# Performance work log

Hardware: AMD Instinct MI355X
Metric: run time of the kernel (lower is better)

Reference implementation:

```python
import jax, jax.numpy as jnp
import numpy as np

B, S, D, H, HD = 2, 2048, 2048, 16, 128
MAX_TIMESCALE = 10000.0


def _fixed_pos_embedding(features, length, max_timescale):
    # flaxformer embedding.generate_fixed_pos_embedding
    fraction = jnp.arange(0, features, 2, dtype=jnp.float32) / features
    timescale = max_timescale ** fraction  # min_timescale = 1.0
    sinusoid = jnp.einsum('i,j->ij', jnp.arange(length, dtype=jnp.float32), 1.0 / timescale)
    sinusoid = jnp.concatenate([sinusoid, sinusoid], axis=-1)  # [length, features]
    return jnp.sin(sinusoid), jnp.cos(sinusoid)


def _rotate_half(x):
    x1, x2 = jnp.split(x, 2, axis=-1)
    return jnp.concatenate([-x2, x1], axis=-1)


def _apply_rope(x, sin, cos):
    # x: [B, S, H, HD]; sin/cos: [S, HD]
    sin = sin[None, :, None, :].astype(x.dtype)
    cos = cos[None, :, None, :].astype(x.dtype)
    return x * cos + _rotate_half(x) * sin


def setup_inputs() -> dict:
    key = jax.random.key(0)
    ks = jax.random.split(key, 6)
    inputs_q = jax.random.normal(ks[0], (B, S, D), dtype=jnp.float32)
    inputs_kv = jax.random.normal(ks[1], (B, S, D), dtype=jnp.float32)
    scale = D ** -0.5
    wq = jax.random.normal(ks[2], (D, H, HD), dtype=jnp.float32) * scale
    wk = jax.random.normal(ks[3], (D, H, HD), dtype=jnp.float32) * scale
    wv = jax.random.normal(ks[4], (D, H, HD), dtype=jnp.float32) * scale
    wo = jax.random.normal(ks[5], (H, HD, D), dtype=jnp.float32) * ((H * HD) ** -0.5)
    mask = jnp.tril(jnp.ones((S, S), dtype=bool))[None, None]  # causal [1,1,S,S]
    return {"inputs_q": inputs_q, "inputs_kv": inputs_kv, "wq": wq, "wk": wk,
            "wv": wv, "wo": wo, "mask": mask}


def reference(inputs_q, inputs_kv, wq, wk, wv, wo, mask):
    # QKV projections (split-head kernels) -> [B, S, H, HD]
    q = jnp.einsum('bqd,dhf->bqhf', inputs_q, wq)
    k = jnp.einsum('bkd,dhf->bkhf', inputs_kv, wk)
    v = jnp.einsum('bkd,dhf->bkhf', inputs_kv, wv)

    # Rotary embeddings applied to full head dim (fraction_to_rotate = 1.0)
    sin, cos = _fixed_pos_embedding(HD, S, MAX_TIMESCALE)
    q = _apply_rope(q, sin, cos)
    k = _apply_rope(k, sin, cos)

    # Logit rescaling by 1/sqrt(head_dim) (rescale_logits=False default path)
    q = q * (HD ** -0.5)

    logits = jnp.einsum('bqhf,bkhf->bhqk', q, k)  # [B, H, S, S]
    logits = jnp.where(mask, logits, jnp.asarray(-1e10, logits.dtype))
    probs = jax.nn.softmax(logits, axis=-1)

    ctx = jnp.einsum('bhqk,bkhf->bqhf', probs, v)
    out = jnp.einsum('bqhf,hfd->bqd', ctx, wo)  # output projection
    return out
```

## Files before the change

### kernel.cpp

```cpp
#include <hip/hip_runtime.h>

#define S_LEN 2048
#define NH 16
#define HDIM 128
#define DMODEL 2048

typedef __attribute__((ext_vector_type(8))) short bf16x8;
typedef __attribute__((ext_vector_type(4))) float f32x4;

using gas_cvp = const __attribute__((address_space(1))) void*;
using las_vp  = __attribute__((address_space(3))) void*;

__device__ __forceinline__ unsigned short f2bf(float x) {
  unsigned int u = __builtin_bit_cast(unsigned int, x);
  u += 0x7FFFu + ((u >> 16) & 1u);
  return (unsigned short)(u >> 16);
}
__device__ __forceinline__ float bf2f(unsigned short u) {
  unsigned int x = ((unsigned int)u) << 16;
  return __builtin_bit_cast(float, x);
}
__device__ __forceinline__ unsigned int cvt_pk_bf16(float lo, float hi) {
  unsigned int r;
  asm("v_cvt_pk_bf16_f32 %0, %1, %2" : "=v"(r) : "v"(lo), "v"(hi));
  return r;
}

__global__ __launch_bounds__(256) void cvt_kernel(const float4* __restrict__ in,
                                                  ushort4* __restrict__ out, int n4) {
  int i = blockIdx.x * 256 + threadIdx.x;
  if (i < n4) {
    float4 v = in[i];
    ushort4 r;
    r.x = f2bf(v.x); r.y = f2bf(v.y); r.z = f2bf(v.z); r.w = f2bf(v.w);
    out[i] = r;
  }
}

__global__ __launch_bounds__(256) void sincos_kernel(float2* __restrict__ sc) {
  int i = blockIdx.x * 256 + threadIdx.x;
  int s = i >> 6, j = i & 63;
  float inv_ts = 1.0f / powf(10000.0f, (float)j * (1.0f / 64.0f));
  float ang = (float)s * inv_ts;
  sc[i] = make_float2(sinf(ang), cosf(ang));
}

__global__ __launch_bounds__(256) void rope8_kernel(const unsigned short* __restrict__ XQ,
                                                    const unsigned short* __restrict__ XK,
                                                    const float2* __restrict__ sc,
                                                    unsigned short* __restrict__ outQ,
                                                    unsigned short* __restrict__ outK,
                                                    float qscale) {
  const unsigned short* X = blockIdx.z ? XK : XQ;
  unsigned short* out = blockIdx.z ? outK : outQ;
  float scale = blockIdx.z ? 1.0f : qscale;
  int i = blockIdx.x * 256 + threadIdx.x;
  int m = i >> 7;
  int r = i & 127;
  int h = r >> 3, jb = (r & 7) * 8;
  int s = m & (S_LEN - 1);
  size_t base = (size_t)m * DMODEL + h * HDIM + jb;
  int4 x1 = *(const int4*)(X + base);
  int4 x2 = *(const int4*)(X + base + 64);
  const float2* pp = sc + s * 64 + jb;
  int4 o1, o2;
  int* x1w = (int*)&x1; int* x2w = (int*)&x2;
  int* o1w = (int*)&o1; int* o2w = (int*)&o2;
#pragma unroll
  for (int w = 0; w < 4; w++) {
    float a_lo = bf2f((unsigned short)(x1w[w] & 0xffff));
    float a_hi = bf2f((unsigned short)((unsigned int)x1w[w] >> 16));
    float b_lo = bf2f((unsigned short)(x2w[w] & 0xffff));
    float b_hi = bf2f((unsigned short)((unsigned int)x2w[w] >> 16));
    float2 c0 = pp[w * 2], c1 = pp[w * 2 + 1];
    float r1l = (a_lo * c0.y - b_lo * c0.x) * scale;
    float r1h = (a_hi * c1.y - b_hi * c1.x) * scale;
    float r2l = (b_lo * c0.y + a_lo * c0.x) * scale;
    float r2h = (b_hi * c1.y + a_hi * c1.x) * scale;
    o1w[w] = (int)(cvt_pk_bf16(r1l, r1h));
    o2w[w] = (int)(cvt_pk_bf16(r2l, r2h));
  }
  *(int4*)(out + base) = o1;
  *(int4*)(out + base + 64) = o2;
}

__global__ __launch_bounds__(256) void wtrans4_kernel(const float* __restrict__ w0,
                                                      const float* __restrict__ w1,
                                                      const float* __restrict__ w2,
                                                      const float* __restrict__ w3,
                                                      unsigned short* __restrict__ outb) {
  __shared__ float tile[64][65];
  int z = blockIdx.z;
  const float* in = (z == 0) ? w0 : (z == 1) ? w1 : (z == 2) ? w2 : w3;
  unsigned short* out = outb + (size_t)z * DMODEL * DMODEL;
  int c0 = blockIdx.x * 64, r0 = blockIdx.y * 64;
  int tx = threadIdx.x & 63, ty = threadIdx.x >> 6;
#pragma unroll
  for (int i = 0; i < 16; i++) {
    int r = ty + i * 4;
    tile[r][tx] = in[(size_t)(r0 + r) * DMODEL + c0 + tx];
  }
  __syncthreads();
#pragma unroll
  for (int i = 0; i < 16; i++) {
    int c = ty + i * 4;
    out[(size_t)(c0 + c) * DMODEL + r0 + tx] = f2bf(tile[tx][c]);
  }
}

__global__ __launch_bounds__(256) void vtrans_kernel(const unsigned short* __restrict__ vf,
                                                     unsigned short* __restrict__ Vt) {
  __shared__ unsigned short tile[64][65];
  int z = blockIdx.z; int b = z >> 4, h = z & 15;
  const unsigned short* I = vf + (size_t)b * S_LEN * DMODEL + h * HDIM;
  unsigned short* O = Vt + (size_t)z * HDIM * S_LEN;
  int s0 = blockIdx.y * 64, f0 = blockIdx.x * 64;
  int tx = threadIdx.x & 63, ty = threadIdx.x >> 6;
#pragma unroll
  for (int i = 0; i < 16; i++) {
    int r = ty + i * 4;
    tile[r][tx] = I[(size_t)(s0 + r) * DMODEL + f0 + tx];
  }
  __syncthreads();
#pragma unroll
  for (int i = 0; i < 16; i++) {
    int c = ty + i * 4;
    O[(size_t)(f0 + c) * S_LEN + s0 + tx] = tile[tx][c];
  }
}

template <bool BF16OUT>
__global__ __launch_bounds__(512, 2) void gemm256_kernel(
    const unsigned short* __restrict__ Aq,
    const unsigned short* __restrict__ Akv,
    const unsigned short* __restrict__ W,
    void* __restrict__ Cb) {
  constexpr int M = 4096, N = 2048, K = 2048, NT = K / 64;
  __shared__ char lds[131072];
  int z = blockIdx.z;
  const unsigned short* A = (z == 0) ? Aq : Akv;
  const unsigned short* Bt = W + (size_t)z * N * K;

  int wid = blockIdx.y * 8 + blockIdx.x;
  int nid = (wid & 7) * 16 + (wid >> 3);
  int bn = (nid & 7) * 256, bm = (nid >> 3) * 256;

  int tid = threadIdx.x, wave = tid >> 6, lane = tid & 63;
  int lr = lane & 15, lq = lane >> 4;
  int wr = wave >> 2, wc = wave & 3;

  auto STAGE_Q = [&](int t, int buf, int isB, int q) {
    int k0 = (t & (NT - 1)) * 64;
    const unsigned short* src = isB ? Bt : A;
    int rbase = (isB ? bn : bm) + q * 64;
    int o = tid * 16;
    int row = o >> 7, colb = o & 127;
    int sc = colb ^ ((row & 7) << 4);
    __builtin_amdgcn_global_load_lds(
        (gas_cvp)(src + (size_t)(rbase + row) * K + k0 + (sc >> 1)),
        (las_vp)(lds + buf * 65536 + isB * 32768 + (q >> 1) * 16384 + (q & 1) * 8192 + wave * 1024),
        16, 0, 0);
  };
  auto STAGE_AA = [&](int t, int buf) { STAGE_Q(t, buf, 0, 0); STAGE_Q(t, buf, 0, 2); };
  auto STAGE_BIG = [&](int t, int buf) {
    STAGE_Q(t, buf, 0, 1); STAGE_Q(t, buf, 0, 3);
    STAGE_Q(t, buf, 1, 0); STAGE_Q(t, buf, 1, 1);
    STAGE_Q(t, buf, 1, 2); STAGE_Q(t, buf, 1, 3);
  };

  auto LDA = [&](int buf, int m, int kk) -> bf16x8 {
    int row = wr * 128 + m * 16 + lr;
    int half = row >> 7, r = row & 127;
    return *(const bf16x8*)(lds + buf * 65536 + half * 16384 + r * 128 +
                            (((kk * 4 + lq) ^ (r & 7)) << 4));
  };
  auto LDB = [&](int buf, int n, int kk) -> bf16x8 {
    int row = wc * 64 + n * 16 + lr;
    int half = row >> 7, r = row & 127;
    return *(const bf16x8*)(lds + buf * 65536 + 32768 + half * 16384 + r * 128 +
                            (((kk * 4 + lq) ^ (r & 7)) << 4));
  };

  f32x4 acc[8][4] = {};
  bf16x8 aA[4][2], bB[4][2];

  auto DS_A = [&](int buf, int mg) {
#pragma unroll
    for (int kk = 0; kk < 2; kk++)
#pragma unroll
      for (int mm = 0; mm < 4; mm++) aA[mm][kk] = LDA(buf, mg * 4 + mm, kk);
  };
  auto DS_B = [&](int buf, int ng) {
#pragma unroll
    for (int kk = 0; kk < 2; kk++)
#pragma unroll
      for (int nn = 0; nn < 2; nn++) bB[ng * 2 + nn][kk] = LDB(buf, ng * 2 + nn, kk);
  };
  auto MFMA_Q = [&](int mg, int ng) {
#pragma unroll
    for (int kk = 0; kk < 2; kk++)
#pragma unroll
      for (int mm = 0; mm < 4; mm++)
#pragma unroll
        for (int nn = 0; nn < 2; nn++)
          acc[mg * 4 + mm][ng * 2 + nn] = __builtin_amdgcn_mfma_f32_16x16x32_bf16(
              aA[mm][kk], bB[ng * 2 + nn][kk], acc[mg * 4 + mm][ng * 2 + nn], 0, 0, 0);
  };
  auto PH_MID = [&]() {
    __builtin_amdgcn_s_barrier();
    asm volatile("s_waitcnt lgkmcnt(0)" ::: "memory");
    __builtin_amdgcn_sched_barrier(0);
    __builtin_amdgcn_s_setprio(1);
  };
  auto PH_ENDP = [&]() {
    __builtin_amdgcn_s_setprio(0);
    __builtin_amdgcn_s_barrier();
  };
  auto PH_END_VM2 = [&]() {
    __builtin_amdgcn_s_setprio(0);
    asm volatile("s_waitcnt vmcnt(2)" ::: "memory");
    __builtin_amdgcn_sched_barrier(0);
    __builtin_amdgcn_s_barrier();
  };

  STAGE_AA(0, 0); STAGE_BIG(0, 0);
  STAGE_AA(1, 1);
  asm volatile("s_waitcnt vmcnt(2)" ::: "memory");
  __builtin_amdgcn_sched_barrier(0);
  __builtin_amdgcn_s_barrier();

  for (int i = 0; i < NT / 2; i++) {
    int T = 2 * i, U = T + 1;
    int t2 = (T + 2) & (NT - 1), u2 = (U + 2) & (NT - 1);
    DS_A(0, 0); DS_B(0, 0);
    STAGE_BIG(U, 1);
    PH_MID(); MFMA_Q(0, 0); PH_ENDP();
    DS_B(0, 1);
    PH_MID(); MFMA_Q(0, 1); PH_ENDP();
    DS_A(0, 1);
    STAGE_AA(t2, 0);
    PH_MID(); MFMA_Q(1, 0); PH_ENDP();
    PH_MID(); MFMA_Q(1, 1); PH_END_VM2();
    DS_A(1, 0); DS_B(1, 0);
    STAGE_BIG(t2, 0);
    PH_MID(); MFMA_Q(0, 0); PH_ENDP();
    DS_B(1, 1);
    PH_MID(); MFMA_Q(0, 1); PH_ENDP();
    DS_A(1, 1);
    STAGE_AA(u2, 1);
    PH_MID(); MFMA_Q(1, 0); PH_ENDP();
    PH_MID(); MFMA_Q(1, 1); PH_END_VM2();
  }
  asm volatile("s_waitcnt vmcnt(0)" ::: "memory");

#pragma unroll
  for (int m = 0; m < 8; m++)
#pragma unroll
    for (int n = 0; n < 4; n++) {
      int row0 = bm + wr * 128 + m * 16 + lq * 4;
      int col = bn + wc * 64 + n * 16 + lr;
      if (BF16OUT) {
        unsigned short* C = (unsigned short*)Cb + (size_t)z * M * N;
#pragma unroll
        for (int r = 0; r < 4; r++)
          C[(size_t)(row0 + r) * N + col] = f2bf(acc[m][n][r]);
      } else {
        float* C = (float*)Cb + (size_t)z * M * N;
#pragma unroll
        for (int r = 0; r < 4; r++)
          C[(size_t)(row0 + r) * N + col] = acc[m][n][r];
      }
    }
}

__global__ __launch_bounds__(512, 1) void attn_kernel(const unsigned short* __restrict__ Qb,
                                                      const unsigned short* __restrict__ Kb,
                                                      const unsigned short* __restrict__ Vt,
                                                      unsigned short* __restrict__ ctx) {
  __shared__ char lds[65536];
  int d = blockIdx.x + 8 * (blockIdx.y + 16 * blockIdx.z);
  int jlo = (d >> 3) & 7;
  int hb = (d & 7) * 4 + (d >> 6);
  int h = hb & 15, b = hb >> 4;

  int tid = threadIdx.x, wave = tid >> 6, lane = tid & 63;
  int lr = lane & 15, lq = lane >> 4;
  int grp = wave >> 2, wsub = wave & 3;
  int qtile = grp ? (15 - jlo) : jlo;
  int qw = qtile * 128 + wsub * 32;
  int nt = 2 * (15 - jlo) + 2;

  const unsigned short* Qp = Qb + (size_t)b * S_LEN * DMODEL + (size_t)h * HDIM;
  const unsigned short* Kp = Kb + (size_t)b * S_LEN * DMODEL + (size_t)h * HDIM;
  const unsigned short* Vp = Vt + (size_t)(b * NH + h) * HDIM * S_LEN;

  bf16x8 qa[2][4];
#pragma unroll
  for (int mi = 0; mi < 2; mi++)
#pragma unroll
    for (int kf = 0; kf < 4; kf++)
      qa[mi][kf] = *(const bf16x8*)(Qp + (size_t)(qw + mi * 16 + lr) * DMODEL + kf * 32 + lq * 8);

  f32x4 o[2][8] = {};
  float mrow[2] = {-1e30f, -1e30f};
  float lsum[2] = {0.f, 0.f};

  auto STAGE = [&](int tt, int bsel) {
    int kk0 = tt * 64;
#pragma unroll
    for (int i = 0; i < 2; i++) {
      int o_ = wave * 2048 + i * 1024 + lane * 16;
      int row = o_ >> 8, colb = o_ & 255;
      int sc_ = colb ^ ((row & 7) << 4);
      __builtin_amdgcn_global_load_lds(
          (gas_cvp)(Kp + (size_t)(kk0 + row) * DMODEL + (sc_ >> 1)),
          (las_vp)(lds + bsel * 32768 + wave * 2048 + i * 1024), 16, 0, 0);
    }
#pragma unroll
    for (int i = 0; i < 2; i++) {
      int o_ = wave * 2048 + i * 1024 + lane * 16;
      int row = o_ >> 7, colb = o_ & 127;
      int sc_ = colb ^ ((row & 7) << 4);
      __builtin_amdgcn_global_load_lds(
          (gas_cvp)(Vp + (size_t)row * S_LEN + kk0 + (sc_ >> 1)),
          (las_vp)(lds + bsel * 32768 + 16384 + wave * 2048 + i * 1024), 16, 0, 0);
    }
  };

  STAGE(0, 0);
  __syncthreads();

  for (int t = 0; t < nt; t++) {
    int cur = t & 1;
    int k0 = t * 64;
    if (t + 1 < nt) STAGE(t + 1, cur ^ 1);

    bool active = (k0 <= qw + 31);
    if (active) {
      const char* kbb = lds + cur * 32768;
      f32x4 sf[2][4] = {};
#pragma unroll
      for (int kf = 0; kf < 4; kf++) {
        bf16x8 kbf[4];
#pragma unroll
        for (int nf = 0; nf < 4; nf++) {
          int row = nf * 16 + lr;
          int colb = kf * 64 + lq * 16;
          kbf[nf] = *(const bf16x8*)(kbb + row * 256 + (colb ^ ((row & 7) << 4)));
        }
#pragma unroll
        for (int nf = 0; nf < 4; nf++)
#pragma unroll
          for (int mi = 0; mi < 2; mi++)
            sf[mi][nf] = __builtin_amdgcn_mfma_f32_16x16x32_bf16(kbf[nf], qa[mi][kf], sf[mi][nf], 0, 0, 0);
      }

      if (k0 + 63 > qw) {
#pragma unroll
        for (int mi = 0; mi < 2; mi++) {
          int q = qw + mi * 16 + lr;
#pragma unroll
          for (int nf = 0; nf < 4; nf++)
#pragma unroll
            for (int r = 0; r < 4; r++)
              if (k0 + nf * 16 + lq * 4 + r > q) sf[mi][nf][r] = -1e30f;
        }
      }

      float vmax[2];
#pragma unroll
      for (int mi = 0; mi < 2; mi++) {
        float v = sf[mi][0][0];
#pragma unroll
        for (int nf = 0; nf < 4; nf++)
#pragma unroll
          for (int r = 0; r < 4; r++) v = fmaxf(v, sf[mi][nf][r]);
        v = fmaxf(v, __shfl_xor(v, 16));
        v = fmaxf(v, __shfl_xor(v, 32));
        vmax[mi] = v;
      }
      bool need = (vmax[0] > mrow[0] + 8.f) || (vmax[1] > mrow[1] + 8.f);
      if (__any(need)) {
#pragma unroll
        for (int mi = 0; mi < 2; mi++) {
          float mn = fmaxf(mrow[mi], vmax[mi]);
          float al = __expf(mrow[mi] - mn);
          mrow[mi] = mn;
          lsum[mi] *= al;
#pragma unroll
          for (int ff = 0; ff < 8; ff++) o[mi][ff] *= al;
        }
      }
#pragma unroll
      for (int mi = 0; mi < 2; mi++) {
        float rs = 0.f;
#pragma unroll
        for (int nf = 0; nf < 4; nf++)
#pragma unroll
          for (int r = 0; r < 4; r++) {
            float p = __expf(sf[mi][nf][r] - mrow[mi]);
            sf[mi][nf][r] = p;
            rs += p;
          }
        rs += __shfl_xor(rs, 16);
        rs += __shfl_xor(rs, 32);
        lsum[mi] += rs;
      }

      const char* vbb = lds + cur * 32768 + 16384;
      bool hi = (lane >= 32);
      bool odd = (lq & 1);
#pragma unroll
      for (int c = 0; c < 2; c++) {
        bf16x8 pfrag[2];
#pragma unroll
        for (int mi = 0; mi < 2; mi++) {
          unsigned int A0 = cvt_pk_bf16(sf[mi][2 * c][0], sf[mi][2 * c][1]);
          unsigned int A1 = cvt_pk_bf16(sf[mi][2 * c][2], sf[mi][2 * c][3]);
          unsigned int B0 = cvt_pk_bf16(sf[mi][2 * c + 1][0], sf[mi][2 * c + 1][1]);
          unsigned int B1 = cvt_pk_bf16(sf[mi][2 * c + 1][2], sf[mi][2 * c + 1][3]);
          unsigned int sA0 = (unsigned int)__shfl_xor((int)A0, 32);
          unsigned int sA1 = (unsigned int)__shfl_xor((int)A1, 32);
          unsigned int sB0 = (unsigned int)__shfl_xor((int)B0, 32);
          unsigned int sB1 = (unsigned int)__shfl_xor((int)B1, 32);
          unsigned int Y0f = hi ? sB0 : A0, Y0s = hi ? B0 : sA0;
          unsigned int Y1f = hi ? sB1 : A1, Y1s = hi ? B1 : sA1;
          unsigned int z0 = odd ? Y0f : Y0s, z1 = odd ? Y1f : Y1s;
          unsigned int w0 = (unsigned int)__shfl_xor((int)z0, 16);
          unsigned int w1 = (unsigned int)__shfl_xor((int)z1, 16);
          int4 fr;
          fr.x = (int)(odd ? w0 : Y0f);
          fr.y = (int)(odd ? w1 : Y1f);
          fr.z = (int)(odd ? Y0s : w0);
          fr.w = (int)(odd ? Y1s : w1);
          pfrag[mi] = __builtin_bit_cast(bf16x8, fr);
        }
#pragma unroll
        for (int ff = 0; ff < 8; ff++) {
          int row = ff * 16 + lr;
          int colb = c * 64 + lq * 16;
          bf16x8 vb = *(const bf16x8*)(vbb + row * 128 + (colb ^ ((row & 7) << 4)));
#pragma unroll
          for (int mi = 0; mi < 2; mi++)
            o[mi][ff] = __builtin_amdgcn_mfma_f32_16x16x32_bf16(vb, pfrag[mi], o[mi][ff], 0, 0, 0);
        }
      }
    }

    __syncthreads();
  }

#pragma unroll
  for (int mi = 0; mi < 2; mi++) {
    float inv = 1.0f / lsum[mi];
    size_t rb = ((size_t)b * S_LEN + qw + mi * 16 + lr) * DMODEL + h * HDIM;
#pragma unroll
    for (int ff = 0; ff < 8; ff++) {
      unsigned int u0 = cvt_pk_bf16(o[mi][ff][0] * inv, o[mi][ff][1] * inv);
      unsigned int u1 = cvt_pk_bf16(o[mi][ff][2] * inv, o[mi][ff][3] * inv);
      *(uint2*)(ctx + rb + ff * 16 + lq * 4) = make_uint2(u0, u1);
    }
  }
}

extern "C" void kernel_launch(void* const* d_in, const int* in_sizes, int n_in,
                              void* d_out, int out_size, void* d_ws, size_t ws_size,
                              hipStream_t stream) {
  const float* inq  = (const float*)d_in[0];
  const float* inkv = (const float*)d_in[1];
  const float* wq   = (const float*)d_in[2];
  const float* wk   = (const float*)d_in[3];
  const float* wv   = (const float*)d_in[4];
  const float* wo   = (const float*)d_in[5];
  float* out = (float*)d_out;

  char* ws = (char*)d_ws;
  const size_t MB = 1ull << 20;
  unsigned short* xq  = (unsigned short*)(ws);
  unsigned short* xkv = (unsigned short*)(ws + 16 * MB);
  unsigned short* wqt = (unsigned short*)(ws + 32 * MB);
  unsigned short* wot = (unsigned short*)(ws + 56 * MB);
  float2* sc          = (float2*)(ws + 64 * MB);
  unsigned short* projb = (unsigned short*)(ws + 66 * MB);
  unsigned short* Vt   = (unsigned short*)(ws + 114 * MB);
  unsigned short* ctxb = (unsigned short*)(ws + 130 * MB);
  unsigned short* Qb = xq;
  unsigned short* Kb = xkv;

  const int n4 = (2 * S_LEN * DMODEL) / 4;
  cvt_kernel<<<n4 / 256, 256, 0, stream>>>((const float4*)inq, (ushort4*)xq, n4);
  cvt_kernel<<<n4 / 256, 256, 0, stream>>>((const float4*)inkv, (ushort4*)xkv, n4);

  wtrans4_kernel<<<dim3(32, 32, 4), 256, 0, stream>>>(wq, wk, wv, wo, wqt);

  sincos_kernel<<<(S_LEN * 64) / 256, 256, 0, stream>>>(sc);

  const float qscale = 0.08838834764831845f;
  unsigned short* projQ = projb;
  unsigned short* projK = projb + (size_t)4096 * 2048;
  unsigned short* projV = projb + (size_t)2 * 4096 * 2048;

  gemm256_kernel<true><<<dim3(8, 16, 3), 512, 0, stream>>>(xq, xkv, wqt, (void*)projb);

  rope8_kernel<<<dim3(2048, 1, 2), 256, 0, stream>>>(projQ, projK, sc, Qb, Kb, qscale);
  vtrans_kernel<<<dim3(2, 32, 32), 256, 0, stream>>>(projV, Vt);

  attn_kernel<<<dim3(8, NH, 2), 512, 0, stream>>>(Qb, Kb, Vt, ctxb);

  gemm256_kernel<false><<<dim3(8, 16, 1), 512, 0, stream>>>(ctxb, ctxb, wot, (void*)out);
}
```

Baseline: 302.0 us.

## Switch projection GEMMs to 256x128 tiles with 4-wave ping-pong pipeline

```diff
diff --git a/kernel.cpp b/kernel.cpp
--- a/kernel.cpp
+++ b/kernel.cpp
@@ -130,73 +130,75 @@
 }
 
 template <bool BF16OUT>
-__global__ __launch_bounds__(512, 2) void gemm256_kernel(
+__global__ __launch_bounds__(256, 1) void gemmp_kernel(
     const unsigned short* __restrict__ Aq,
     const unsigned short* __restrict__ Akv,
     const unsigned short* __restrict__ W,
     void* __restrict__ Cb) {
   constexpr int M = 4096, N = 2048, K = 2048, NT = K / 64;
-  __shared__ char lds[131072];
+  __shared__ char lds[98304];
   int z = blockIdx.z;
   const unsigned short* A = (z == 0) ? Aq : Akv;
   const unsigned short* Bt = W + (size_t)z * N * K;
 
-  int wid = blockIdx.y * 8 + blockIdx.x;
-  int nid = (wid & 7) * 16 + (wid >> 3);
-  int bn = (nid & 7) * 256, bm = (nid >> 3) * 256;
+  int wid = blockIdx.y * 16 + blockIdx.x;
+  int nid = (wid & 7) * 32 + (wid >> 3);
+  int bn = (nid & 15) * 128, bm = (nid >> 4) * 256;
 
   int tid = threadIdx.x, wave = tid >> 6, lane = tid & 63;
   int lr = lane & 15, lq = lane >> 4;
-  int wr = wave >> 2, wc = wave & 3;
-
-  auto STAGE_Q = [&](int t, int buf, int isB, int q) {
+  int wr = wave >> 1, wc = wave & 1;
+
+  auto STAGE_A_MG = [&](int t, int buf, int mg) {
     int k0 = (t & (NT - 1)) * 64;
-    const unsigned short* src = isB ? Bt : A;
-    int rbase = (isB ? bn : bm) + q * 64;
-    int o = tid * 16;
-    int row = o >> 7, colb = o & 127;
-    int sc = colb ^ ((row & 7) << 4);
-    __builtin_amdgcn_global_load_lds(
-        (gas_cvp)(src + (size_t)(rbase + row) * K + k0 + (sc >> 1)),
-        (las_vp)(lds + buf * 65536 + isB * 32768 + (q >> 1) * 16384 + (q & 1) * 8192 + wave * 1024),
-        16, 0, 0);
+#pragma unroll
+    for (int i = 0; i < 4; i++) {
+      int o = i * 4096 + wave * 1024 + lane * 16;
+      int rr = o >> 7, colb = o & 127;
+      int sc = colb ^ ((rr & 7) << 4);
+      int grow = bm + ((rr >> 6) << 7) + mg * 64 + (rr & 63);
+      __builtin_amdgcn_global_load_lds(
+          (gas_cvp)(A + (size_t)grow * K + k0 + (sc >> 1)),
+          (las_vp)(lds + buf * 49152 + mg * 16384 + i * 4096 + wave * 1024), 16, 0, 0);
+    }
   };
-  auto STAGE_AA = [&](int t, int buf) { STAGE_Q(t, buf, 0, 0); STAGE_Q(t, buf, 0, 2); };
-  auto STAGE_BIG = [&](int t, int buf) {
-    STAGE_Q(t, buf, 0, 1); STAGE_Q(t, buf, 0, 3);
-    STAGE_Q(t, buf, 1, 0); STAGE_Q(t, buf, 1, 1);
-    STAGE_Q(t, buf, 1, 2); STAGE_Q(t, buf, 1, 3);
+  auto STAGE_B = [&](int t, int buf) {
+    int k0 = (t & (NT - 1)) * 64;
+#pragma unroll
+    for (int i = 0; i < 4; i++) {
+      int o = i * 4096 + wave * 1024 + lane * 16;
+      int rr = o >> 7, colb = o & 127;
+      int sc = colb ^ ((rr & 7) << 4);
+      __builtin_amdgcn_global_load_lds(
+          (gas_cvp)(Bt + (size_t)(bn + rr) * K + k0 + (sc >> 1)),
+          (las_vp)(lds + buf * 49152 + 32768 + i * 4096 + wave * 1024), 16, 0, 0);
+    }
   };
 
-  auto LDA = [&](int buf, int m, int kk) -> bf16x8 {
-    int row = wr * 128 + m * 16 + lr;
-    int half = row >> 7, r = row & 127;
-    return *(const bf16x8*)(lds + buf * 65536 + half * 16384 + r * 128 +
-                            (((kk * 4 + lq) ^ (r & 7)) << 4));
+  bf16x8 aS0[4][2], aS1[4][2], bS0[2][2], bS1[2][2];
+  f32x4 acc[8][4] = {};
+
+  auto RD_A = [&](int buf, int mg, bf16x8 (&dst)[4][2]) {
+#pragma unroll
+    for (int kk = 0; kk < 2; kk++)
+#pragma unroll
+      for (int mm = 0; mm < 4; mm++) {
+        int rr = wr * 64 + mm * 16 + lr;
+        dst[mm][kk] = *(const bf16x8*)(lds + buf * 49152 + mg * 16384 + rr * 128 +
+                                       (((kk * 4 + lq) ^ (rr & 7)) << 4));
+      }
   };
-  auto LDB = [&](int buf, int n, int kk) -> bf16x8 {
-    int row = wc * 64 + n * 16 + lr;
-    int half = row >> 7, r = row & 127;
-    return *(const bf16x8*)(lds + buf * 65536 + 32768 + half * 16384 + r * 128 +
-                            (((kk * 4 + lq) ^ (r & 7)) << 4));
+  auto RD_Bn = [&](int buf, int ng, bf16x8 (&dst)[2][2]) {
+#pragma unroll
+    for (int kk = 0; kk < 2; kk++)
+#pragma unroll
+      for (int nn = 0; nn < 2; nn++) {
+        int rr = wc * 64 + (ng * 2 + nn) * 16 + lr;
+        dst[nn][kk] = *(const bf16x8*)(lds + buf * 49152 + 32768 + rr * 128 +
+                                       (((kk * 4 + lq) ^ (rr & 7)) << 4));
+      }
   };
-
-  f32x4 acc[8][4] = {};
-  bf16x8 aA[4][2], bB[4][2];
-
-  auto DS_A = [&](int buf, int mg) {
-#pragma unroll
-    for (int kk = 0; kk < 2; kk++)
-#pragma unroll
-      for (int mm = 0; mm < 4; mm++) aA[mm][kk] = LDA(buf, mg * 4 + mm, kk);
-  };
-  auto DS_B = [&](int buf, int ng) {
-#pragma unroll
-    for (int kk = 0; kk < 2; kk++)
-#pragma unroll
-      for (int nn = 0; nn < 2; nn++) bB[ng * 2 + nn][kk] = LDB(buf, ng * 2 + nn, kk);
-  };
-  auto MFMA_Q = [&](int mg, int ng) {
+  auto MFMA_Q = [&](int mg, int ng, bf16x8 (&aS)[4][2], bf16x8 (&bS)[2][2]) {
 #pragma unroll
     for (int kk = 0; kk < 2; kk++)
 #pragma unroll
@@ -204,54 +206,48 @@
 #pragma unroll
         for (int nn = 0; nn < 2; nn++)
           acc[mg * 4 + mm][ng * 2 + nn] = __builtin_amdgcn_mfma_f32_16x16x32_bf16(
-              aA[mm][kk], bB[ng * 2 + nn][kk], acc[mg * 4 + mm][ng * 2 + nn], 0, 0, 0);
+              aS[mm][kk], bS[nn][kk], acc[mg * 4 + mm][ng * 2 + nn], 0, 0, 0);
   };
-  auto PH_MID = [&]() {
+
+  STAGE_A_MG(0, 0, 0); STAGE_A_MG(0, 0, 1); STAGE_B(0, 0);
+  STAGE_B(1, 1);
+  asm volatile("s_waitcnt vmcnt(4)" ::: "memory");
+  __builtin_amdgcn_sched_barrier(0);
+  __builtin_amdgcn_s_barrier();
+  RD_A(0, 0, aS0); RD_Bn(0, 0, bS0);
+  __builtin_amdgcn_sched_barrier(0);
+
+  for (int X = 0; X < NT; X++) {
+    int c = X & 1, nc = c ^ 1;
+    RD_Bn(c, 1, bS1);
+    __builtin_amdgcn_sched_barrier(0);
+    STAGE_A_MG(X + 1, nc, 0);
+    asm volatile("s_waitcnt lgkmcnt(4)" ::: "memory");
+    __builtin_amdgcn_sched_barrier(0);
+    MFMA_Q(0, 0, aS0, bS0);
+    __builtin_amdgcn_s_barrier();
+    RD_A(c, 1, aS1);
+    __builtin_amdgcn_sched_barrier(0);
+    STAGE_A_MG(X + 1, nc, 1);
+    asm volatile("s_waitcnt lgkmcnt(8)" ::: "memory");
+    __builtin_amdgcn_sched_barrier(0);
+    MFMA_Q(0, 1, aS0, bS1);
     __builtin_amdgcn_s_barrier();
     asm volatile("s_waitcnt lgkmcnt(0)" ::: "memory");
     __builtin_amdgcn_sched_barrier(0);
-    __builtin_amdgcn_s_setprio(1);
-  };
-  auto PH_ENDP = [&]() {
-    __builtin_amdgcn_s_setprio(0);
+    MFMA_Q(1, 0, aS1, bS0);
+    asm volatile("s_waitcnt vmcnt(4)" ::: "memory");
+    __builtin_amdgcn_sched_barrier(0);
     __builtin_amdgcn_s_barrier();
-  };
-  auto PH_END_VM2 = [&]() {
-    __builtin_amdgcn_s_setprio(0);
-    asm volatile("s_waitcnt vmcnt(2)" ::: "memory");
+    RD_A(nc, 0, aS0); RD_Bn(nc, 0, bS0);
+    __builtin_amdgcn_sched_barrier(0);
+    STAGE_B(X + 2, c);
+    MFMA_Q(1, 1, aS1, bS1);
+    asm volatile("s_waitcnt vmcnt(4)" ::: "memory");
     __builtin_amdgcn_sched_barrier(0);
     __builtin_amdgcn_s_barrier();
-  };
-
-  STAGE_AA(0, 0); STAGE_BIG(0, 0);
-  STAGE_AA(1, 1);
-  asm volatile("s_waitcnt vmcnt(2)" ::: "memory");
-  __builtin_amdgcn_sched_barrier(0);
-  __builtin_amdgcn_s_barrier();
-
-  for (int i = 0; i < NT / 2; i++) {
-    int T = 2 * i, U = T + 1;
-    int t2 = (T + 2) & (NT - 1), u2 = (U + 2) & (NT - 1);
-    DS_A(0, 0); DS_B(0, 0);
-    STAGE_BIG(U, 1);
-    PH_MID(); MFMA_Q(0, 0); PH_ENDP();
-    DS_B(0, 1);
-    PH_MID(); MFMA_Q(0, 1); PH_ENDP();
-    DS_A(0, 1);
-    STAGE_AA(t2, 0);
-    PH_MID(); MFMA_Q(1, 0); PH_ENDP();
-    PH_MID(); MFMA_Q(1, 1); PH_END_VM2();
-    DS_A(1, 0); DS_B(1, 0);
-    STAGE_BIG(t2, 0);
-    PH_MID(); MFMA_Q(0, 0); PH_ENDP();
-    DS_B(1, 1);
-    PH_MID(); MFMA_Q(0, 1); PH_ENDP();
-    DS_A(1, 1);
-    STAGE_AA(u2, 1);
-    PH_MID(); MFMA_Q(1, 0); PH_ENDP();
-    PH_MID(); MFMA_Q(1, 1); PH_END_VM2();
-  }
-  asm volatile("s_waitcnt vmcnt(0)" ::: "memory");
+  }
+  asm volatile("s_waitcnt vmcnt(0) lgkmcnt(0)" ::: "memory");
 
 #pragma unroll
   for (int m = 0; m < 8; m++)
@@ -500,12 +496,12 @@
   unsigned short* projK = projb + (size_t)4096 * 2048;
   unsigned short* projV = projb + (size_t)2 * 4096 * 2048;
 
-  gemm256_kernel<true><<<dim3(8, 16, 3), 512, 0, stream>>>(xq, xkv, wqt, (void*)projb);
+  gemmp_kernel<true><<<dim3(16, 16, 3), 256, 0, stream>>>(xq, xkv, wqt, (void*)projb);
 
   rope8_kernel<<<dim3(2048, 1, 2), 256, 0, stream>>>(projQ, projK, sc, Qb, Kb, qscale);
   vtrans_kernel<<<dim3(2, 32, 32), 256, 0, stream>>>(projV, Vt);
 
   attn_kernel<<<dim3(8, NH, 2), 512, 0, stream>>>(Qb, Kb, Vt, ctxb);
 
-  gemm256_kernel<false><<<dim3(8, 16, 1), 512, 0, stream>>>(ctxb, ctxb, wot, (void*)out);
-}
+  gemmp_kernel<false><<<dim3(16, 16, 1), 256, 0, stream>>>(ctxb, ctxb, wot, (void*)out);
+}
```

Measured after the change: 304.5 us. No clear change (+0.8%).
